# Performance work log

Measured on AMD Instinct MI355X. Metric: run time of the kernel, lower is better.

The kernel has to match this reference:

```python
import jax, jax.numpy as jnp
import numpy as np

N, A, R = 131072, 16, 64


def setup_inputs() -> dict:
    key = jax.random.key(0)
    k1, k2, k3 = jax.random.split(key, 3)
    x = jax.random.normal(k1, (N, A), dtype=jnp.float32)
    mu = jax.random.uniform(k2, (R, A), dtype=jnp.float32)      # torch.rand(R, A)
    sigma = jnp.ones((R, A), dtype=jnp.float32) * 0.2           # torch.ones(R, A) * 0.2
    rho = jax.random.normal(k3, (R, A + 1), dtype=jnp.float32) * 0.1
    return {"x": x, "mu": mu, "sigma": sigma, "rho": rho}


def reference(x, mu, sigma, rho):
    # Rule consequents: z[k, r] = x[k] . rho[r, :A] + rho[r, A]   -> [N, R]
    z = jnp.einsum("na,ra->nr", x, rho[:, :-1]) + rho[:, -1]
    # Gaussian membership firing strengths (prod of exps == exp of sum):
    # w[k, r] = prod_a exp(-(x[k,a]-mu[r,a])^2 / (2 sigma[r,a]^2))
    d = x[:, None, :] - mu[None, :, :]                           # [N, R, A]
    logw = -jnp.sum(d * d / (2.0 * sigma[None] ** 2), axis=-1)   # [N, R]
    w = jnp.exp(logw)
    # diag(z @ w.T)[k] = sum_r z[k,r] * w[k,r]; normalized by rule-sum.
    num = jnp.sum(z * w, axis=1)
    den = jnp.sum(w, axis=1) + 1e-13
    return num / den
```

## Files before the change

kernel.cpp:

```cpp
#include <hip/hip_runtime.h>
#include <hip/hip_bf16.h>
#include <math.h>

#define NFEAT 16
#define NRULE 64
#define RSTRIDE 52
#define RPW 16
#define WPB 4

__constant__ float CST[NRULE * RSTRIDE];

__global__ void fuzzy_prep(const float* __restrict__ mu,
                           const float* __restrict__ sigma,
                           const float* __restrict__ rho,
                           float* __restrict__ cst) {
    const float L2E = 1.4426950408889634f;
    int r = threadIdx.x;
    if (r >= NRULE) return;
    float* c = cst + r * RSTRIDE;
    float K = 0.0f;
#pragma unroll
    for (int a = 0; a < NFEAT; ++a) {
        float m = mu[r * NFEAT + a];
        float s = sigma[r * NFEAT + a];
        float inv = 1.0f / (2.0f * s * s);
        c[a]      = -inv * L2E;
        c[16 + a] = 2.0f * inv * m * L2E;
        c[32 + a] = rho[r * (NFEAT + 1) + a];
        K         = fmaf(-inv * m, m, K);
    }
    c[48] = rho[r * (NFEAT + 1) + NFEAT];
    c[49] = K * L2E;
    c[50] = 0.0f;
    c[51] = 0.0f;
}

__global__ __launch_bounds__(256) void fuzzy_main(const float* __restrict__ x,
                                                  float* __restrict__ out,
                                                  int n) {
    int lane = threadIdx.x & 63;
    int q    = __builtin_amdgcn_readfirstlane(threadIdx.x >> 6);
    int k    = blockIdx.x * 64 + lane;
    int kc   = k < n ? k : n - 1;

    const float4* x4 = (const float4*)(x + (size_t)kc * NFEAT);
    float4 v0 = x4[0], v1 = x4[1], v2 = x4[2], v3 = x4[3];
    float xs[NFEAT] = {v0.x, v0.y, v0.z, v0.w,
                       v1.x, v1.y, v1.z, v1.w,
                       v2.x, v2.y, v2.z, v2.w,
                       v3.x, v3.y, v3.z, v3.w};
    float xq[NFEAT];
#pragma unroll
    for (int a = 0; a < NFEAT; ++a) xq[a] = xs[a] * xs[a];

    float num = 0.0f, den = 0.0f;
    const float* cbase = CST + q * (RPW * RSTRIDE);
#pragma unroll 4
    for (int r = 0; r < RPW; ++r) {
        const float* c = cbase + r * RSTRIDE;
        float z  = c[48];
        float l0 = c[49];
        float l1 = 0.0f;
#pragma unroll
        for (int a = 0; a < NFEAT; ++a) {
            z  = fmaf(c[32 + a], xs[a], z);
            l0 = fmaf(c[a],      xq[a], l0);
            l1 = fmaf(c[16 + a], xs[a], l1);
        }
        float w = __builtin_amdgcn_exp2f(l0 + l1);
        num = fmaf(z, w, num);
        den += w;
    }

    __shared__ float pnum[WPB][64];
    __shared__ float pden[WPB][64];
    pnum[q][lane] = num;
    pden[q][lane] = den;
    __syncthreads();
    if (q == 0 && k < n) {
        float nn = pnum[0][lane] + pnum[1][lane] + pnum[2][lane] + pnum[3][lane];
        float dd = pden[0][lane] + pden[1][lane] + pden[2][lane] + pden[3][lane];
        out[k] = nn / (dd + 1e-13f);
    }
}

extern "C" void kernel_launch(void* const* d_in, const int* in_sizes, int n_in,
                              void* d_out, int out_size, void* d_ws, size_t ws_size,
                              hipStream_t stream) {
    const float* x     = (const float*)d_in[0];
    const float* mu    = (const float*)d_in[1];
    const float* sigma = (const float*)d_in[2];
    const float* rho   = (const float*)d_in[3];
    float* out = (float*)d_out;

    int n = in_sizes[0] / NFEAT;

    void* cst_dev = nullptr;
    (void)hipGetSymbolAddress(&cst_dev, HIP_SYMBOL(CST));

    fuzzy_prep<<<1, 64, 0, stream>>>(mu, sigma, rho, (float*)cst_dev);
    fuzzy_main<<<(n + 63) / 64, 256, 0, stream>>>(x, out, n);
}
```

Measured before the change: 75.45 us.

## Stage rule constants in LDS via workspace and factor the quadratic with FMAs

Rule coefficients now live in a workspace buffer instead of __constant__ memory. Each block copies them into shared memory as float4s and reads them back with vector LDS loads rather than scalar constant loads. The inner loop evaluates the quadratic as (n*x+m)*x, which drops the precomputed x^2 array, and the unroll factor goes from 4 to 2. The cost is a per-block copy of all 64 rules' constants plus a barrier, even though each wave uses only 16 rules. LDS reads also replace scalar/SGPR operands, adding VGPR pressure.

```diff
diff --git a/kernel.cpp b/kernel.cpp
--- a/kernel.cpp
+++ b/kernel.cpp
@@ -4,11 +4,9 @@
 
 #define NFEAT 16
 #define NRULE 64
-#define RSTRIDE 52
+#define RQUADS 13
 #define RPW 16
 #define WPB 4
-
-__constant__ float CST[NRULE * RSTRIDE];
 
 __global__ void fuzzy_prep(const float* __restrict__ mu,
                            const float* __restrict__ sigma,
@@ -17,7 +15,7 @@
     const float L2E = 1.4426950408889634f;
     int r = threadIdx.x;
     if (r >= NRULE) return;
-    float* c = cst + r * RSTRIDE;
+    float* c = cst + r * (RQUADS * 4);
     float K = 0.0f;
 #pragma unroll
     for (int a = 0; a < NFEAT; ++a) {
@@ -36,12 +34,25 @@
 }
 
 __global__ __launch_bounds__(256) void fuzzy_main(const float* __restrict__ x,
+                                                  const float* __restrict__ cst,
                                                   float* __restrict__ out,
                                                   int n) {
-    int lane = threadIdx.x & 63;
-    int q    = __builtin_amdgcn_readfirstlane(threadIdx.x >> 6);
-    int k    = blockIdx.x * 64 + lane;
-    int kc   = k < n ? k : n - 1;
+    __shared__ float4 cl[NRULE * RQUADS];
+    __shared__ float pnum[WPB][64];
+    __shared__ float pden[WPB][64];
+
+    const int tid  = threadIdx.x;
+    const int lane = tid & 63;
+    const int q    = __builtin_amdgcn_readfirstlane(tid >> 6);
+    const int k    = blockIdx.x * 64 + lane;
+    const int kc   = k < n ? k : n - 1;
+
+    const float4* cg = (const float4*)cst;
+#pragma unroll
+    for (int i = 0; i < 4; ++i) {
+        int idx = tid + i * 256;
+        if (idx < NRULE * RQUADS) cl[idx] = cg[idx];
+    }
 
     const float4* x4 = (const float4*)(x + (size_t)kc * NFEAT);
     float4 v0 = x4[0], v1 = x4[1], v2 = x4[2], v3 = x4[3];
@@ -49,31 +60,40 @@
                        v1.x, v1.y, v1.z, v1.w,
                        v2.x, v2.y, v2.z, v2.w,
                        v3.x, v3.y, v3.z, v3.w};
-    float xq[NFEAT];
-#pragma unroll
-    for (int a = 0; a < NFEAT; ++a) xq[a] = xs[a] * xs[a];
+
+    __syncthreads();
 
     float num = 0.0f, den = 0.0f;
-    const float* cbase = CST + q * (RPW * RSTRIDE);
-#pragma unroll 4
+    const float4* cb = cl + q * (RPW * RQUADS);
+#pragma unroll 2
     for (int r = 0; r < RPW; ++r) {
-        const float* c = cbase + r * RSTRIDE;
-        float z  = c[48];
-        float l0 = c[49];
-        float l1 = 0.0f;
+        const float4* c = cb + r * RQUADS;
+        float4 n0 = c[0], n1 = c[1], n2 = c[2], n3 = c[3];
+        float4 m0 = c[4], m1 = c[5], m2 = c[6], m3 = c[7];
+        float4 r0 = c[8], r1 = c[9], r2 = c[10], r3 = c[11];
+        float4 tl = c[12];
+        float nc[NFEAT]  = {n0.x,n0.y,n0.z,n0.w, n1.x,n1.y,n1.z,n1.w,
+                            n2.x,n2.y,n2.z,n2.w, n3.x,n3.y,n3.z,n3.w};
+        float cm[NFEAT]  = {m0.x,m0.y,m0.z,m0.w, m1.x,m1.y,m1.z,m1.w,
+                            m2.x,m2.y,m2.z,m2.w, m3.x,m3.y,m3.z,m3.w};
+        float rh[NFEAT]  = {r0.x,r0.y,r0.z,r0.w, r1.x,r1.y,r1.z,r1.w,
+                            r2.x,r2.y,r2.z,r2.w, r3.x,r3.y,r3.z,r3.w};
+        float z  = tl.x;
+        float l0 = tl.y, l1 = 0.0f;
 #pragma unroll
-        for (int a = 0; a < NFEAT; ++a) {
-            z  = fmaf(c[32 + a], xs[a], z);
-            l0 = fmaf(c[a],      xq[a], l0);
-            l1 = fmaf(c[16 + a], xs[a], l1);
+        for (int a = 0; a < NFEAT; a += 2) {
+            float t0 = fmaf(nc[a],     xs[a],     cm[a]);
+            float t1 = fmaf(nc[a + 1], xs[a + 1], cm[a + 1]);
+            l0 = fmaf(t0, xs[a],     l0);
+            l1 = fmaf(t1, xs[a + 1], l1);
+            z  = fmaf(rh[a],     xs[a],     z);
+            z  = fmaf(rh[a + 1], xs[a + 1], z);
         }
         float w = __builtin_amdgcn_exp2f(l0 + l1);
         num = fmaf(z, w, num);
         den += w;
     }
 
-    __shared__ float pnum[WPB][64];
-    __shared__ float pden[WPB][64];
     pnum[q][lane] = num;
     pden[q][lane] = den;
     __syncthreads();
@@ -92,12 +112,10 @@
     const float* sigma = (const float*)d_in[2];
     const float* rho   = (const float*)d_in[3];
     float* out = (float*)d_out;
+    float* cst = (float*)d_ws;
 
     int n = in_sizes[0] / NFEAT;
 
-    void* cst_dev = nullptr;
-    (void)hipGetSymbolAddress(&cst_dev, HIP_SYMBOL(CST));
-
-    fuzzy_prep<<<1, 64, 0, stream>>>(mu, sigma, rho, (float*)cst_dev);
-    fuzzy_main<<<(n + 63) / 64, 256, 0, stream>>>(x, out, n);
+    fuzzy_prep<<<1, 64, 0, stream>>>(mu, sigma, rho, cst);
+    fuzzy_main<<<(n + 63) / 64, 256, 0, stream>>>(x, cst, out, n);
 }
```

After: 77.61 us. 2.9% more time.
